# Optimization experiments

Measured on AMD Instinct MI355X. Metric: run time of the kernel, lower is better.

The kernel has to match this reference:

```python
import jax, jax.numpy as jnp
import numpy as np

N = 100000
D = 64
H = 4 * D  # 256
E = 1000000


def setup_inputs() -> dict:
    key = jax.random.key(0)
    ks = jax.random.split(key, 9)
    return {
        "loc_feat": jax.random.normal(ks[0], (N, D), dtype=jnp.float32),
        "geo_src": jax.random.randint(ks[1], (E,), 0, N),
        "geo_dst": jax.random.randint(ks[2], (E,), 0, N),
        "trans_src": jax.random.randint(ks[3], (E,), 0, N),
        "trans_dst": jax.random.randint(ks[4], (E,), 0, N),
        "trans_w": jax.random.uniform(ks[5], (E,), dtype=jnp.float32),
        "W1": jax.random.normal(ks[6], (D, H), dtype=jnp.float32) * (1.0 / np.sqrt(D)),
        "b1": jax.random.normal(ks[7], (H,), dtype=jnp.float32) * 0.01,
        "W2": jax.random.normal(ks[8], (H, 1), dtype=jnp.float32) * (1.0 / np.sqrt(H)),
    }


def reference(loc_feat, geo_src, geo_dst, trans_src, trans_dst, trans_w, W1, b1, W2):
    n = loc_feat.shape[0]
    # etype 'geo': copy_u + mean  -> segment mean of src features at dst
    geo_sum = jax.ops.segment_sum(loc_feat[geo_src], geo_dst, num_segments=n)
    cnt = jax.ops.segment_sum(jnp.ones(geo_src.shape[0], loc_feat.dtype), geo_dst, num_segments=n)
    geo = jnp.where(cnt[:, None] > 0, geo_sum / jnp.maximum(cnt, 1.0)[:, None], 0.0)
    # etype 'trans': u_mul_e + sum -> weighted segment sum
    trans = jax.ops.segment_sum(loc_feat[trans_src] * trans_w[:, None], trans_dst, num_segments=n)
    # semantic attention fuse over the two relation views
    z = jnp.stack([geo, trans], axis=1)          # [N, 2, D]
    h = jnp.tanh(jnp.einsum('nkd,dh->nkh', z, W1) + b1)  # [N, 2, H]
    w = jnp.einsum('nkh,ho->nko', h, W2).mean(0)  # [2, 1] (mean over nodes)
    beta = jax.nn.softmax(w, axis=0)              # [2, 1]
    return (beta[None, :, :] * z).sum(1)          # [N, D]
```

## Files before the change

### kernel.cpp

```cpp
#include <hip/hip_runtime.h>
#include <hip/hip_bf16.h>

#define N_NODES 100000
#define DIM 64
#define HID 256
#define E_EDGES 1000000
#define TWO_N (2 * N_NODES)
#define MLP_ROWBLOCKS (TWO_N / 64)

#define TILE 120
#define NBINS 834
#define CAP 1600
#define EPB 4096
#define FILL_BLOCKS 245
#define FEAT_BLOCKS ((N_NODES * DIM / 4) / 256)

typedef short short8 __attribute__((ext_vector_type(8)));
typedef float f32x4 __attribute__((ext_vector_type(4)));
typedef unsigned short us4 __attribute__((ext_vector_type(4)));

__device__ __forceinline__ float tanh_fast(float x) {
    x = fminf(fmaxf(x, -15.0f), 15.0f);
    float e = __expf(2.0f * x);
    return (e - 1.0f) / (e + 1.0f);
}

__device__ __forceinline__ unsigned short f2bf(float x) {
    unsigned u = __float_as_uint(x);
    u = u + 0x7FFFu + ((u >> 16) & 1u);
    return (unsigned short)(u >> 16);
}

__device__ __forceinline__ float bf2f(unsigned short u) {
    return __uint_as_float(((unsigned)u) << 16);
}

__global__ void pack_kernel(const float* __restrict__ feat, unsigned short* __restrict__ fb,
                            const float* __restrict__ W1, unsigned short* __restrict__ W1p) {
    int b = blockIdx.x;
    if (b < FEAT_BLOCKS) {
        int i = b * 256 + threadIdx.x;
        float4 v = ((const float4*)feat)[i];
        us4 o;
        o[0] = f2bf(v.x); o[1] = f2bf(v.y); o[2] = f2bf(v.z); o[3] = f2bf(v.w);
        ((us4*)fb)[i] = o;
    } else {
        for (int i = threadIdx.x; i < 16384; i += 256) {
            int j = i & 7;
            int r = i >> 3;
            int nidx = r & 15; r >>= 4;
            int q = r & 3; r >>= 2;
            int khalf = r & 1;
            int n = r >> 1;
            int k = 32 * khalf + 8 * q + j;
            int c = 16 * n + nidx;
            W1p[i] = f2bf(W1[k * HID + c]);
        }
    }
}

__global__ void __launch_bounds__(512) bin_fill_kernel(
        const int* __restrict__ gs, const int* __restrict__ gd,
        const int* __restrict__ ts, const int* __restrict__ td,
        const float* __restrict__ tw,
        int* __restrict__ gcount,
        int* __restrict__ gbin, int2* __restrict__ tbin) {
    __shared__ int   hist[NBINS];
    __shared__ int   adjS[NBINS];
    __shared__ int   curS[NBINS];
    __shared__ int   pS[EPB];
    __shared__ float w2S[EPB];
    __shared__ unsigned short binS[EPB];
    __shared__ int   wsumS[8];

    int t = threadIdx.x, lane = t & 63, wid = t >> 6;
    int blk = blockIdx.x;
    int rel = (blk >= FILL_BLOCKS) ? 1 : 0;
    int e0 = (rel ? blk - FILL_BLOCKS : blk) * EPB;
    const int* dstp = rel ? td : gd;
    const int* srcp = rel ? ts : gs;

    for (int i = t; i < NBINS; i += 512) hist[i] = 0;
    __syncthreads();

    int d_[8], s_[8];
    float w_[8];
    #pragma unroll
    for (int j = 0; j < 2; ++j) {
        int idx = e0 + j * 2048 + 4 * t;
        if (idx + 3 < E_EDGES) {
            int4 dv = *(const int4*)&dstp[idx];
            int4 sv = *(const int4*)&srcp[idx];
            d_[4*j+0] = dv.x; d_[4*j+1] = dv.y; d_[4*j+2] = dv.z; d_[4*j+3] = dv.w;
            s_[4*j+0] = sv.x; s_[4*j+1] = sv.y; s_[4*j+2] = sv.z; s_[4*j+3] = sv.w;
            if (rel) {
                float4 wv = *(const float4*)&tw[idx];
                w_[4*j+0] = wv.x; w_[4*j+1] = wv.y; w_[4*j+2] = wv.z; w_[4*j+3] = wv.w;
            }
        } else {
            #pragma unroll
            for (int i2 = 0; i2 < 4; ++i2) {
                bool ok = (idx + i2 < E_EDGES);
                d_[4*j+i2] = ok ? dstp[idx + i2] : -1;
                s_[4*j+i2] = ok ? srcp[idx + i2] : 0;
                w_[4*j+i2] = (ok && rel) ? tw[idx + i2] : 0.0f;
            }
        }
    }
    #pragma unroll
    for (int i = 0; i < 8; ++i)
        if (d_[i] >= 0) atomicAdd(&hist[d_[i] / TILE], 1);
    __syncthreads();

    int b0i = 2 * t, b1i = 2 * t + 1;
    int h0 = (b0i < NBINS) ? hist[b0i] : 0;
    int h1 = (b1i < NBINS) ? hist[b1i] : 0;
    int c = h0 + h1;
    int v = c;
    #pragma unroll
    for (int off = 1; off < 64; off <<= 1) {
        int u = __shfl_up(v, off);
        if (lane >= off) v += u;
    }
    if (lane == 63) wsumS[wid] = v;
    __syncthreads();
    if (t == 0) {
        int run = 0;
        #pragma unroll
        for (int i = 0; i < 8; ++i) { int x = wsumS[i]; wsumS[i] = run; run += x; }
    }
    __syncthreads();
    int excl = v - c + wsumS[wid];
    if (b0i < NBINS) {
        curS[b0i] = excl;
        int gb = (h0 > 0) ? (b0i * CAP + atomicAdd(&gcount[rel * NBINS + b0i], h0)) : 0;
        adjS[b0i] = gb - excl;
    }
    if (b1i < NBINS) {
        int lb1 = excl + h0;
        curS[b1i] = lb1;
        int gb = (h1 > 0) ? (b1i * CAP + atomicAdd(&gcount[rel * NBINS + b1i], h1)) : 0;
        adjS[b1i] = gb - lb1;
    }
    __syncthreads();

    #pragma unroll
    for (int i = 0; i < 8; ++i) {
        int d = d_[i];
        if (d < 0) continue;
        int bin = d / TILE;
        int pos = atomicAdd(&curS[bin], 1);
        pS[pos] = s_[i] | ((d - bin * TILE) << 20);
        binS[pos] = (unsigned short)bin;
        if (rel) w2S[pos] = w_[i];
    }
    __syncthreads();

    int nV = min(EPB, E_EDGES - e0);
    if (!rel) {
        for (int i = t; i < nV; i += 512) {
            int b = binS[i];
            int gi = adjS[b] + i;
            if (gi < (b + 1) * CAP)
                gbin[gi] = pS[i];
        }
    } else {
        for (int i = t; i < nV; i += 512) {
            int b = binS[i];
            int gi = adjS[b] + i;
            if (gi < (b + 1) * CAP)
                tbin[gi] = make_int2(pS[i], __float_as_int(w2S[i]));
        }
    }
}

__global__ void __launch_bounds__(256) aggregate_kernel(
        const unsigned short* __restrict__ featb,
        const int* __restrict__ gbin, const int2* __restrict__ tbin,
        const int* __restrict__ gcount,
        unsigned short* __restrict__ zb) {
    __shared__ int   srcS[CAP];
    __shared__ float wS[CAP];
    __shared__ int   histS[TILE];
    __shared__ int   baseS[TILE];
    __shared__ int   curS[TILE];
    __shared__ int   w0sum[1];

    int b = blockIdx.x;
    int rel = (b >= NBINS) ? 1 : 0;
    int bin = rel ? b - NBINS : b;
    int node0 = bin * TILE;
    int nNodes = min(TILE, N_NODES - node0);
    int t = threadIdx.x, lane = t & 63, wave = t >> 6;
    int q = lane >> 4, ql = lane & 15;

    int nE = gcount[b];
    if (nE > CAP) nE = CAP;

    for (int i = t; i < TILE; i += 256) histS[i] = 0;
    __syncthreads();

    if (!rel) {
        const int* bp = gbin + (size_t)bin * CAP;
        for (int i = t; i < nE; i += 256) atomicAdd(&histS[bp[i] >> 20], 1);
    } else {
        const int2* bp = tbin + (size_t)bin * CAP;
        for (int i = t; i < nE; i += 256) atomicAdd(&histS[bp[i].x >> 20], 1);
    }
    __syncthreads();

    int h = (t < TILE) ? histS[t] : 0;
    int v = h;
    #pragma unroll
    for (int off = 1; off < 64; off <<= 1) {
        int u = __shfl_up(v, off);
        if (lane >= off) v += u;
    }
    if (t == 63) w0sum[0] = v;
    __syncthreads();
    if (wave == 1) v += w0sum[0];
    if (t < TILE) {
        int base = v - h;
        baseS[t] = base;
        curS[t] = base;
    }
    __syncthreads();

    if (!rel) {
        const int* bp = gbin + (size_t)bin * CAP;
        for (int i = t; i < nE; i += 256) {
            int p = bp[i];
            int pos = atomicAdd(&curS[p >> 20], 1);
            srcS[pos] = p & 0xFFFFF;
        }
    } else {
        const int2* bp = tbin + (size_t)bin * CAP;
        for (int i = t; i < nE; i += 256) {
            int2 p = bp[i];
            int pos = atomicAdd(&curS[p.x >> 20], 1);
            srcS[pos] = p.x & 0xFFFFF;
            wS[pos] = __int_as_float(p.y);
        }
    }
    __syncthreads();

    for (int nl0 = wave * 4; nl0 < nNodes; nl0 += 16) {
        int nl = nl0 + q;
        bool act = (nl < nNodes);
        int deg = act ? histS[nl] : 0;
        int base = act ? baseS[nl] : 0;
        float a0 = 0.f, a1 = 0.f, a2 = 0.f, a3 = 0.f;
        if (!rel) {
            int k = 0;
            for (; k + 7 < deg; k += 8) {
                int s0 = srcS[base + k],     s1 = srcS[base + k + 1];
                int s2 = srcS[base + k + 2], s3 = srcS[base + k + 3];
                int s4 = srcS[base + k + 4], s5 = srcS[base + k + 5];
                int s6 = srcS[base + k + 6], s7 = srcS[base + k + 7];
                us4 r0 = *(const us4*)&featb[(size_t)s0 * DIM + ql * 4];
                us4 r1 = *(const us4*)&featb[(size_t)s1 * DIM + ql * 4];
                us4 r2 = *(const us4*)&featb[(size_t)s2 * DIM + ql * 4];
                us4 r3 = *(const us4*)&featb[(size_t)s3 * DIM + ql * 4];
                us4 r4 = *(const us4*)&featb[(size_t)s4 * DIM + ql * 4];
                us4 r5 = *(const us4*)&featb[(size_t)s5 * DIM + ql * 4];
                us4 r6 = *(const us4*)&featb[(size_t)s6 * DIM + ql * 4];
                us4 r7 = *(const us4*)&featb[(size_t)s7 * DIM + ql * 4];
                a0 += ((bf2f(r0[0]) + bf2f(r1[0])) + (bf2f(r2[0]) + bf2f(r3[0])))
                    + ((bf2f(r4[0]) + bf2f(r5[0])) + (bf2f(r6[0]) + bf2f(r7[0])));
                a1 += ((bf2f(r0[1]) + bf2f(r1[1])) + (bf2f(r2[1]) + bf2f(r3[1])))
                    + ((bf2f(r4[1]) + bf2f(r5[1])) + (bf2f(r6[1]) + bf2f(r7[1])));
                a2 += ((bf2f(r0[2]) + bf2f(r1[2])) + (bf2f(r2[2]) + bf2f(r3[2])))
                    + ((bf2f(r4[2]) + bf2f(r5[2])) + (bf2f(r6[2]) + bf2f(r7[2])));
                a3 += ((bf2f(r0[3]) + bf2f(r1[3])) + (bf2f(r2[3]) + bf2f(r3[3])))
                    + ((bf2f(r4[3]) + bf2f(r5[3])) + (bf2f(r6[3]) + bf2f(r7[3])));
            }
            for (; k + 1 < deg; k += 2) {
                int s0 = srcS[base + k], s1 = srcS[base + k + 1];
                us4 r0 = *(const us4*)&featb[(size_t)s0 * DIM + ql * 4];
                us4 r1 = *(const us4*)&featb[(size_t)s1 * DIM + ql * 4];
                a0 += bf2f(r0[0]) + bf2f(r1[0]);
                a1 += bf2f(r0[1]) + bf2f(r1[1]);
                a2 += bf2f(r0[2]) + bf2f(r1[2]);
                a3 += bf2f(r0[3]) + bf2f(r1[3]);
            }
            if (k < deg) {
                int s = srcS[base + k];
                us4 r = *(const us4*)&featb[(size_t)s * DIM + ql * 4];
                a0 += bf2f(r[0]); a1 += bf2f(r[1]);
                a2 += bf2f(r[2]); a3 += bf2f(r[3]);
            }
        } else {
            int k = 0;
            for (; k + 7 < deg; k += 8) {
                int s0 = srcS[base + k],     s1 = srcS[base + k + 1];
                int s2 = srcS[base + k + 2], s3 = srcS[base + k + 3];
                int s4 = srcS[base + k + 4], s5 = srcS[base + k + 5];
                int s6 = srcS[base + k + 6], s7 = srcS[base + k + 7];
                float w0 = wS[base + k],     w1 = wS[base + k + 1];
                float w2 = wS[base + k + 2], w3 = wS[base + k + 3];
                float w4 = wS[base + k + 4], w5 = wS[base + k + 5];
                float w6 = wS[base + k + 6], w7 = wS[base + k + 7];
                us4 r0 = *(const us4*)&featb[(size_t)s0 * DIM + ql * 4];
                us4 r1 = *(const us4*)&featb[(size_t)s1 * DIM + ql * 4];
                us4 r2 = *(const us4*)&featb[(size_t)s2 * DIM + ql * 4];
                us4 r3 = *(const us4*)&featb[(size_t)s3 * DIM + ql * 4];
                us4 r4 = *(const us4*)&featb[(size_t)s4 * DIM + ql * 4];
                us4 r5 = *(const us4*)&featb[(size_t)s5 * DIM + ql * 4];
                us4 r6 = *(const us4*)&featb[(size_t)s6 * DIM + ql * 4];
                us4 r7 = *(const us4*)&featb[(size_t)s7 * DIM + ql * 4];
                a0 += ((bf2f(r0[0])*w0 + bf2f(r1[0])*w1) + (bf2f(r2[0])*w2 + bf2f(r3[0])*w3))
                    + ((bf2f(r4[0])*w4 + bf2f(r5[0])*w5) + (bf2f(r6[0])*w6 + bf2f(r7[0])*w7));
                a1 += ((bf2f(r0[1])*w0 + bf2f(r1[1])*w1) + (bf2f(r2[1])*w2 + bf2f(r3[1])*w3))
                    + ((bf2f(r4[1])*w4 + bf2f(r5[1])*w5) + (bf2f(r6[1])*w6 + bf2f(r7[1])*w7));
                a2 += ((bf2f(r0[2])*w0 + bf2f(r1[2])*w1) + (bf2f(r2[2])*w2 + bf2f(r3[2])*w3))
                    + ((bf2f(r4[2])*w4 + bf2f(r5[2])*w5) + (bf2f(r6[2])*w6 + bf2f(r7[2])*w7));
                a3 += ((bf2f(r0[3])*w0 + bf2f(r1[3])*w1) + (bf2f(r2[3])*w2 + bf2f(r3[3])*w3))
                    + ((bf2f(r4[3])*w4 + bf2f(r5[3])*w5) + (bf2f(r6[3])*w6 + bf2f(r7[3])*w7));
            }
            for (; k + 1 < deg; k += 2) {
                int s0 = srcS[base + k], s1 = srcS[base + k + 1];
                float w0 = wS[base + k], w1 = wS[base + k + 1];
                us4 r0 = *(const us4*)&featb[(size_t)s0 * DIM + ql * 4];
                us4 r1 = *(const us4*)&featb[(size_t)s1 * DIM + ql * 4];
                a0 += bf2f(r0[0]) * w0 + bf2f(r1[0]) * w1;
                a1 += bf2f(r0[1]) * w0 + bf2f(r1[1]) * w1;
                a2 += bf2f(r0[2]) * w0 + bf2f(r1[2]) * w1;
                a3 += bf2f(r0[3]) * w0 + bf2f(r1[3]) * w1;
            }
            if (k < deg) {
                int s = srcS[base + k];
                float w = wS[base + k];
                us4 r = *(const us4*)&featb[(size_t)s * DIM + ql * 4];
                a0 += bf2f(r[0]) * w; a1 += bf2f(r[1]) * w;
                a2 += bf2f(r[2]) * w; a3 += bf2f(r[3]) * w;
            }
        }
        if (act) {
            float sc = rel ? 1.0f : 1.0f / fmaxf((float)deg, 1.0f);
            us4 o;
            o[0] = f2bf(a0 * sc); o[1] = f2bf(a1 * sc);
            o[2] = f2bf(a2 * sc); o[3] = f2bf(a3 * sc);
            size_t row = (size_t)(rel ? N_NODES + node0 + nl : node0 + nl);
            *(us4*)&zb[row * DIM + ql * 4] = o;
        }
    }
}

__global__ void __launch_bounds__(256) mlp_mfma_kernel(
        const unsigned short* __restrict__ zb,
        const unsigned short* __restrict__ W1p,
        const float* __restrict__ bias1, const float* __restrict__ W2,
        float* __restrict__ partials) {
    __shared__ float wred[4][2];
    int t = threadIdx.x, lane = t & 63, wave = t >> 6;
    int m = lane & 15, q = lane >> 4;
    int base = blockIdx.x * 64 + wave * 16;
    int R = base + m;

    const unsigned short* rowp = zb + (size_t)R * DIM;
    short8 a0 = *(const short8*)(rowp + q * 8);
    short8 a1 = *(const short8*)(rowp + 32 + q * 8);

    float c0 = 0.0f, c1 = 0.0f;
    const short8* W1v = (const short8*)W1p;

    #pragma unroll 4
    for (int n = 0; n < 16; ++n) {
        short8 b0 = W1v[(n * 2 + 0) * 64 + lane];
        short8 bK = W1v[(n * 2 + 1) * 64 + lane];
        f32x4 acc = {0.0f, 0.0f, 0.0f, 0.0f};
        acc = __builtin_amdgcn_mfma_f32_16x16x32_bf16(a0, b0, acc, 0, 0, 0);
        acc = __builtin_amdgcn_mfma_f32_16x16x32_bf16(a1, bK, acc, 0, 0, 0);
        int col = 16 * n + m;
        float bj = bias1[col];
        float w2 = W2[col];
        #pragma unroll
        for (int reg = 0; reg < 4; ++reg) {
            int Rr = base + q * 4 + reg;
            float h = tanh_fast(acc[reg] + bj);
            float contrib = h * w2;
            if (Rr < N_NODES) c0 += contrib; else c1 += contrib;
        }
    }

    #pragma unroll
    for (int off = 32; off > 0; off >>= 1) {
        c0 += __shfl_down(c0, off);
        c1 += __shfl_down(c1, off);
    }
    if (lane == 0) { wred[wave][0] = c0; wred[wave][1] = c1; }
    __syncthreads();
    if (t == 0) {
        partials[blockIdx.x * 2 + 0] = wred[0][0] + wred[1][0] + wred[2][0] + wred[3][0];
        partials[blockIdx.x * 2 + 1] = wred[0][1] + wred[1][1] + wred[2][1] + wred[3][1];
    }
}

__global__ void beta_kernel(const float* __restrict__ partials, float* __restrict__ beta) {
    __shared__ float wred[4][2];
    int t = threadIdx.x;
    float c0 = 0.0f, c1 = 0.0f;
    for (int i = t; i < MLP_ROWBLOCKS; i += 256) {
        c0 += partials[i * 2 + 0];
        c1 += partials[i * 2 + 1];
    }
    #pragma unroll
    for (int off = 32; off > 0; off >>= 1) {
        c0 += __shfl_down(c0, off);
        c1 += __shfl_down(c1, off);
    }
    int lane = t & 63, wv = t >> 6;
    if (lane == 0) { wred[wv][0] = c0; wred[wv][1] = c1; }
    __syncthreads();
    if (t == 0) {
        float s0 = (wred[0][0] + wred[1][0] + wred[2][0] + wred[3][0]) / (float)N_NODES;
        float s1 = (wred[0][1] + wred[1][1] + wred[2][1] + wred[3][1]) / (float)N_NODES;
        float m = fmaxf(s0, s1);
        float e0 = __expf(s0 - m), e1 = __expf(s1 - m);
        float inv = 1.0f / (e0 + e1);
        beta[0] = e0 * inv;
        beta[1] = e1 * inv;
    }
}

__global__ void combine_kernel(const unsigned short* __restrict__ zb,
                               const float* __restrict__ beta,
                               float* __restrict__ out) {
    int gid = blockIdx.x * 256 + threadIdx.x;
    float b0 = beta[0];
    float b1 = beta[1];
    uint4 g = *(const uint4*)&zb[(size_t)gid * 8];
    uint4 tr = *(const uint4*)&zb[(size_t)N_NODES * DIM + (size_t)gid * 8];
    float4 o0, o1;
    o0.x = b0 * __uint_as_float(g.x << 16) + b1 * __uint_as_float(tr.x << 16);
    o0.y = b0 * __uint_as_float(g.x & 0xFFFF0000u) + b1 * __uint_as_float(tr.x & 0xFFFF0000u);
    o0.z = b0 * __uint_as_float(g.y << 16) + b1 * __uint_as_float(tr.y << 16);
    o0.w = b0 * __uint_as_float(g.y & 0xFFFF0000u) + b1 * __uint_as_float(tr.y & 0xFFFF0000u);
    o1.x = b0 * __uint_as_float(g.z << 16) + b1 * __uint_as_float(tr.z << 16);
    o1.y = b0 * __uint_as_float(g.z & 0xFFFF0000u) + b1 * __uint_as_float(tr.z & 0xFFFF0000u);
    o1.z = b0 * __uint_as_float(g.w << 16) + b1 * __uint_as_float(tr.w << 16);
    o1.w = b0 * __uint_as_float(g.w & 0xFFFF0000u) + b1 * __uint_as_float(tr.w & 0xFFFF0000u);
    *(float4*)&out[(size_t)gid * 8] = o0;
    *(float4*)&out[(size_t)gid * 8 + 4] = o1;
}

extern "C" void kernel_launch(void* const* d_in, const int* in_sizes, int n_in,
                              void* d_out, int out_size, void* d_ws, size_t ws_size,
                              hipStream_t stream) {
    const float* loc_feat = (const float*)d_in[0];
    const int* geo_src    = (const int*)d_in[1];
    const int* geo_dst    = (const int*)d_in[2];
    const int* trans_src  = (const int*)d_in[3];
    const int* trans_dst  = (const int*)d_in[4];
    const float* trans_w  = (const float*)d_in[5];
    const float* W1       = (const float*)d_in[6];
    const float* b1       = (const float*)d_in[7];
    const float* W2       = (const float*)d_in[8];
    float* out = (float*)d_out;

    int*   gcount   = (int*)d_ws;
    int*   gbin     = gcount + 2 * NBINS;
    int2*  tbin     = (int2*)(gbin + (size_t)NBINS * CAP);
    float* partials = (float*)(tbin + (size_t)NBINS * CAP);
    float* beta     = partials + 2 * MLP_ROWBLOCKS;
    unsigned short* W1p   = (unsigned short*)(beta + 2);
    unsigned short* featb = W1p + 16384;
    unsigned short* zb    = featb + (size_t)N_NODES * DIM;

    hipMemsetAsync(gcount, 0, 2 * NBINS * sizeof(int), stream);

    pack_kernel<<<FEAT_BLOCKS + 1, 256, 0, stream>>>(loc_feat, featb, W1, W1p);
    bin_fill_kernel<<<2 * FILL_BLOCKS, 512, 0, stream>>>(geo_src, geo_dst, trans_src,
                                                         trans_dst, trans_w,
                                                         gcount, gbin, tbin);
    aggregate_kernel<<<2 * NBINS, 256, 0, stream>>>(featb, gbin, tbin, gcount, zb);
    mlp_mfma_kernel<<<MLP_ROWBLOCKS, 256, 0, stream>>>(zb, W1p, b1, W2, partials);
    beta_kernel<<<1, 256, 0, stream>>>(partials, beta);
    combine_kernel<<<(N_NODES * DIM / 8) / 256, 256, 0, stream>>>(zb, beta, out);
}
```

Before: 246.2 us.

## Fuse pack into bin-fill and MLP/beta reduction into aggregation kernel

Merges the bf16 pack kernel into the binning kernel as extra blocks, and fuses the MLP score computation into the aggregation kernel using the just-aggregated rows staged in shared memory. The beta softmax is now computed by the last block through a global atomic ticket, which removes the separate partials and beta kernels. This cuts three launches and a round trip of z through global memory for the MLP. In exchange, each aggregation block uses more shared memory, which can lower occupancy, and the score sums are now order-nondeterministic float atomics.

```diff
diff --git a/kernel.cpp b/kernel.cpp
--- a/kernel.cpp
+++ b/kernel.cpp
@@ -6,18 +6,21 @@
 #define HID 256
 #define E_EDGES 1000000
 #define TWO_N (2 * N_NODES)
-#define MLP_ROWBLOCKS (TWO_N / 64)
 
 #define TILE 120
 #define NBINS 834
 #define CAP 1600
 #define EPB 4096
 #define FILL_BLOCKS 245
-#define FEAT_BLOCKS ((N_NODES * DIM / 4) / 256)
+#define K1_FILL (2 * FILL_BLOCKS)
+#define PACK_BLOCKS 3125
+#define K1_GRID (K1_FILL + 1 + PACK_BLOCKS)
 
 typedef short short8 __attribute__((ext_vector_type(8)));
 typedef float f32x4 __attribute__((ext_vector_type(4)));
 typedef unsigned short us4 __attribute__((ext_vector_type(4)));
+
+#define ZSTRIDE 72
 
 __device__ __forceinline__ float tanh_fast(float x) {
     x = fminf(fmaxf(x, -15.0f), 15.0f);
@@ -35,31 +38,9 @@
     return __uint_as_float(((unsigned)u) << 16);
 }
 
-__global__ void pack_kernel(const float* __restrict__ feat, unsigned short* __restrict__ fb,
-                            const float* __restrict__ W1, unsigned short* __restrict__ W1p) {
-    int b = blockIdx.x;
-    if (b < FEAT_BLOCKS) {
-        int i = b * 256 + threadIdx.x;
-        float4 v = ((const float4*)feat)[i];
-        us4 o;
-        o[0] = f2bf(v.x); o[1] = f2bf(v.y); o[2] = f2bf(v.z); o[3] = f2bf(v.w);
-        ((us4*)fb)[i] = o;
-    } else {
-        for (int i = threadIdx.x; i < 16384; i += 256) {
-            int j = i & 7;
-            int r = i >> 3;
-            int nidx = r & 15; r >>= 4;
-            int q = r & 3; r >>= 2;
-            int khalf = r & 1;
-            int n = r >> 1;
-            int k = 32 * khalf + 8 * q + j;
-            int c = 16 * n + nidx;
-            W1p[i] = f2bf(W1[k * HID + c]);
-        }
-    }
-}
-
-__global__ void __launch_bounds__(512) bin_fill_kernel(
+__global__ void __launch_bounds__(512) prep_kernel(
+        const float* __restrict__ feat, unsigned short* __restrict__ fb,
+        const float* __restrict__ W1, unsigned short* __restrict__ W1p,
         const int* __restrict__ gs, const int* __restrict__ gd,
         const int* __restrict__ ts, const int* __restrict__ td,
         const float* __restrict__ tw,
@@ -74,9 +55,33 @@
     __shared__ int   wsumS[8];
 
     int t = threadIdx.x, lane = t & 63, wid = t >> 6;
-    int blk = blockIdx.x;
-    int rel = (blk >= FILL_BLOCKS) ? 1 : 0;
-    int e0 = (rel ? blk - FILL_BLOCKS : blk) * EPB;
+    int b = blockIdx.x;
+
+    if (b >= K1_FILL + 1) {
+        int i = (b - K1_FILL - 1) * 512 + t;
+        float4 v = ((const float4*)feat)[i];
+        us4 o;
+        o[0] = f2bf(v.x); o[1] = f2bf(v.y); o[2] = f2bf(v.z); o[3] = f2bf(v.w);
+        ((us4*)fb)[i] = o;
+        return;
+    }
+    if (b == K1_FILL) {
+        for (int i = t; i < 16384; i += 512) {
+            int j = i & 7;
+            int r = i >> 3;
+            int nidx = r & 15; r >>= 4;
+            int q = r & 3; r >>= 2;
+            int khalf = r & 1;
+            int n = r >> 1;
+            int k = 32 * khalf + 8 * q + j;
+            int c = 16 * n + nidx;
+            W1p[i] = f2bf(W1[k * HID + c]);
+        }
+        return;
+    }
+
+    int rel = (b >= FILL_BLOCKS) ? 1 : 0;
+    int e0 = (rel ? b - FILL_BLOCKS : b) * EPB;
     const int* dstp = rel ? td : gd;
     const int* srcp = rel ? ts : gs;
 
@@ -159,32 +164,38 @@
     int nV = min(EPB, E_EDGES - e0);
     if (!rel) {
         for (int i = t; i < nV; i += 512) {
-            int b = binS[i];
-            int gi = adjS[b] + i;
-            if (gi < (b + 1) * CAP)
+            int bb = binS[i];
+            int gi = adjS[bb] + i;
+            if (gi < (bb + 1) * CAP)
                 gbin[gi] = pS[i];
         }
     } else {
         for (int i = t; i < nV; i += 512) {
-            int b = binS[i];
-            int gi = adjS[b] + i;
-            if (gi < (b + 1) * CAP)
+            int bb = binS[i];
+            int gi = adjS[bb] + i;
+            if (gi < (bb + 1) * CAP)
                 tbin[gi] = make_int2(pS[i], __float_as_int(w2S[i]));
         }
     }
 }
 
-__global__ void __launch_bounds__(256) aggregate_kernel(
+__global__ void __launch_bounds__(256) agg_mlp_kernel(
         const unsigned short* __restrict__ featb,
         const int* __restrict__ gbin, const int2* __restrict__ tbin,
         const int* __restrict__ gcount,
-        unsigned short* __restrict__ zb) {
+        unsigned short* __restrict__ zb,
+        const unsigned short* __restrict__ W1p,
+        const float* __restrict__ bias1, const float* __restrict__ W2,
+        float* __restrict__ sums, int* __restrict__ ticket,
+        float* __restrict__ beta) {
     __shared__ int   srcS[CAP];
     __shared__ float wS[CAP];
     __shared__ int   histS[TILE];
     __shared__ int   baseS[TILE];
     __shared__ int   curS[TILE];
     __shared__ int   w0sum[1];
+    __shared__ unsigned short zL[128 * ZSTRIDE];
+    __shared__ float wred[4];
 
     int b = blockIdx.x;
     int rel = (b >= NBINS) ? 1 : 0;
@@ -342,84 +353,54 @@
             o[2] = f2bf(a2 * sc); o[3] = f2bf(a3 * sc);
             size_t row = (size_t)(rel ? N_NODES + node0 + nl : node0 + nl);
             *(us4*)&zb[row * DIM + ql * 4] = o;
-        }
-    }
-}
-
-__global__ void __launch_bounds__(256) mlp_mfma_kernel(
-        const unsigned short* __restrict__ zb,
-        const unsigned short* __restrict__ W1p,
-        const float* __restrict__ bias1, const float* __restrict__ W2,
-        float* __restrict__ partials) {
-    __shared__ float wred[4][2];
-    int t = threadIdx.x, lane = t & 63, wave = t >> 6;
-    int m = lane & 15, q = lane >> 4;
-    int base = blockIdx.x * 64 + wave * 16;
-    int R = base + m;
-
-    const unsigned short* rowp = zb + (size_t)R * DIM;
-    short8 a0 = *(const short8*)(rowp + q * 8);
-    short8 a1 = *(const short8*)(rowp + 32 + q * 8);
-
-    float c0 = 0.0f, c1 = 0.0f;
+            *(us4*)&zL[nl * ZSTRIDE + ql * 4] = o;
+        }
+    }
+    __syncthreads();
+
+    int m = lane & 15;
+    float csum = 0.0f;
     const short8* W1v = (const short8*)W1p;
-
-    #pragma unroll 4
-    for (int n = 0; n < 16; ++n) {
-        short8 b0 = W1v[(n * 2 + 0) * 64 + lane];
-        short8 bK = W1v[(n * 2 + 1) * 64 + lane];
-        f32x4 acc = {0.0f, 0.0f, 0.0f, 0.0f};
-        acc = __builtin_amdgcn_mfma_f32_16x16x32_bf16(a0, b0, acc, 0, 0, 0);
-        acc = __builtin_amdgcn_mfma_f32_16x16x32_bf16(a1, bK, acc, 0, 0, 0);
-        int col = 16 * n + m;
-        float bj = bias1[col];
-        float w2 = W2[col];
-        #pragma unroll
-        for (int reg = 0; reg < 4; ++reg) {
-            int Rr = base + q * 4 + reg;
-            float h = tanh_fast(acc[reg] + bj);
-            float contrib = h * w2;
-            if (Rr < N_NODES) c0 += contrib; else c1 += contrib;
-        }
-    }
-
-    #pragma unroll
-    for (int off = 32; off > 0; off >>= 1) {
-        c0 += __shfl_down(c0, off);
-        c1 += __shfl_down(c1, off);
-    }
-    if (lane == 0) { wred[wave][0] = c0; wred[wave][1] = c1; }
+    #pragma unroll
+    for (int tt = 0; tt < 2; ++tt) {
+        int rowbase = (wave * 2 + tt) * 16;
+        short8 fa0 = *(const short8*)&zL[(rowbase + m) * ZSTRIDE + q * 8];
+        short8 fa1 = *(const short8*)&zL[(rowbase + m) * ZSTRIDE + 32 + q * 8];
+        #pragma unroll 4
+        for (int n = 0; n < 16; ++n) {
+            short8 fb0 = W1v[(n * 2 + 0) * 64 + lane];
+            short8 fbK = W1v[(n * 2 + 1) * 64 + lane];
+            f32x4 acc = {0.0f, 0.0f, 0.0f, 0.0f};
+            acc = __builtin_amdgcn_mfma_f32_16x16x32_bf16(fa0, fb0, acc, 0, 0, 0);
+            acc = __builtin_amdgcn_mfma_f32_16x16x32_bf16(fa1, fbK, acc, 0, 0, 0);
+            int col = 16 * n + m;
+            float bj = bias1[col];
+            float w2 = W2[col];
+            #pragma unroll
+            for (int reg = 0; reg < 4; ++reg) {
+                int nl = rowbase + q * 4 + reg;
+                if (nl < nNodes) csum += tanh_fast(acc[reg] + bj) * w2;
+            }
+        }
+    }
+    #pragma unroll
+    for (int off = 32; off > 0; off >>= 1) csum += __shfl_down(csum, off);
+    if (lane == 0) wred[wave] = csum;
     __syncthreads();
     if (t == 0) {
-        partials[blockIdx.x * 2 + 0] = wred[0][0] + wred[1][0] + wred[2][0] + wred[3][0];
-        partials[blockIdx.x * 2 + 1] = wred[0][1] + wred[1][1] + wred[2][1] + wred[3][1];
-    }
-}
-
-__global__ void beta_kernel(const float* __restrict__ partials, float* __restrict__ beta) {
-    __shared__ float wred[4][2];
-    int t = threadIdx.x;
-    float c0 = 0.0f, c1 = 0.0f;
-    for (int i = t; i < MLP_ROWBLOCKS; i += 256) {
-        c0 += partials[i * 2 + 0];
-        c1 += partials[i * 2 + 1];
-    }
-    #pragma unroll
-    for (int off = 32; off > 0; off >>= 1) {
-        c0 += __shfl_down(c0, off);
-        c1 += __shfl_down(c1, off);
-    }
-    int lane = t & 63, wv = t >> 6;
-    if (lane == 0) { wred[wv][0] = c0; wred[wv][1] = c1; }
-    __syncthreads();
-    if (t == 0) {
-        float s0 = (wred[0][0] + wred[1][0] + wred[2][0] + wred[3][0]) / (float)N_NODES;
-        float s1 = (wred[0][1] + wred[1][1] + wred[2][1] + wred[3][1]) / (float)N_NODES;
-        float m = fmaxf(s0, s1);
-        float e0 = __expf(s0 - m), e1 = __expf(s1 - m);
-        float inv = 1.0f / (e0 + e1);
-        beta[0] = e0 * inv;
-        beta[1] = e1 * inv;
+        float cb = wred[0] + wred[1] + wred[2] + wred[3];
+        atomicAdd(&sums[rel], cb);
+        __threadfence();
+        int old = atomicAdd(ticket, 1);
+        if (old == 2 * NBINS - 1) {
+            float s0 = atomicAdd(&sums[0], 0.0f) / (float)N_NODES;
+            float s1 = atomicAdd(&sums[1], 0.0f) / (float)N_NODES;
+            float mx = fmaxf(s0, s1);
+            float e0 = __expf(s0 - mx), e1 = __expf(s1 - mx);
+            float inv = 1.0f / (e0 + e1);
+            beta[0] = e0 * inv;
+            beta[1] = e1 * inv;
+        }
     }
 }
 
@@ -458,23 +439,22 @@
     const float* W2       = (const float*)d_in[8];
     float* out = (float*)d_out;
 
-    int*   gcount   = (int*)d_ws;
-    int*   gbin     = gcount + 2 * NBINS;
-    int2*  tbin     = (int2*)(gbin + (size_t)NBINS * CAP);
-    float* partials = (float*)(tbin + (size_t)NBINS * CAP);
-    float* beta     = partials + 2 * MLP_ROWBLOCKS;
-    unsigned short* W1p   = (unsigned short*)(beta + 2);
+    int*   gcount = (int*)d_ws;
+    float* sums   = (float*)(gcount + 2 * NBINS);
+    int*   ticket = (int*)(sums + 2);
+    float* beta   = (float*)(ticket + 1);
+    int*   gbin   = (int*)(beta + 2);
+    int2*  tbin   = (int2*)(gbin + (size_t)NBINS * CAP);
+    unsigned short* W1p   = (unsigned short*)(tbin + (size_t)NBINS * CAP);
     unsigned short* featb = W1p + 16384;
     unsigned short* zb    = featb + (size_t)N_NODES * DIM;
 
-    hipMemsetAsync(gcount, 0, 2 * NBINS * sizeof(int), stream);
-
-    pack_kernel<<<FEAT_BLOCKS + 1, 256, 0, stream>>>(loc_feat, featb, W1, W1p);
-    bin_fill_kernel<<<2 * FILL_BLOCKS, 512, 0, stream>>>(geo_src, geo_dst, trans_src,
-                                                         trans_dst, trans_w,
-                                                         gcount, gbin, tbin);
-    aggregate_kernel<<<2 * NBINS, 256, 0, stream>>>(featb, gbin, tbin, gcount, zb);
-    mlp_mfma_kernel<<<MLP_ROWBLOCKS, 256, 0, stream>>>(zb, W1p, b1, W2, partials);
-    beta_kernel<<<1, 256, 0, stream>>>(partials, beta);
+    hipMemsetAsync(d_ws, 0, (2 * NBINS + 5) * sizeof(int), stream);
+
+    prep_kernel<<<K1_GRID, 512, 0, stream>>>(loc_feat, featb, W1, W1p,
+                                             geo_src, geo_dst, trans_src, trans_dst,
+                                             trans_w, gcount, gbin, tbin);
+    agg_mlp_kernel<<<2 * NBINS, 256, 0, stream>>>(featb, gbin, tbin, gcount, zb,
+                                                  W1p, b1, W2, sums, ticket, beta);
     combine_kernel<<<(N_NODES * DIM / 8) / 256, 256, 0, stream>>>(zb, beta, out);
 }
```

Result: slower. 264.8 us (+7.5%).
